# Kernel tuning notes

Hardware: AMD Instinct MI355X
Metric: run time of the kernel (lower is better)

The kernel has to match this reference:

```python
import jax, jax.numpy as jnp
import numpy as np

MARGIN = 0.2
LAMBDA_CLS = 1.0
LAMBDA_TRIPLET = 1.0
EPS = 1e-6  # matches torch pairwise_distance eps inside TripletMarginLoss
B, D, C = 8192, 192, 1024


def setup_inputs() -> dict:
    key = jax.random.key(0)
    k1, k2, k3 = jax.random.split(key, 3)
    embeddings = jax.random.normal(k1, (B, D), dtype=jnp.float32)
    logits = jax.random.normal(k2, (B, C), dtype=jnp.float32)
    targets = jax.random.randint(k3, (B,), 0, C, dtype=jnp.int64)
    return {"embeddings": embeddings, "logits": logits, "targets": targets}


def reference(embeddings, logits, targets):
    # ---- classification loss: mean cross entropy ----
    logp = jax.nn.log_softmax(logits, axis=-1)
    cls_loss = -jnp.mean(jnp.take_along_axis(logp, targets[:, None], axis=1))

    # ---- vectorized hard triplet mining (mining='hard'), on detached embeddings ----
    e = jax.lax.stop_gradient(embeddings)
    sq = jnp.sum(e * e, axis=1)                       # [B]
    d2 = sq[:, None] + sq[None, :] - 2.0 * (e @ e.T)  # [B, B]
    dist = jnp.sqrt(jnp.maximum(d2, 0.0))

    same = targets[:, None] == targets[None, :]       # [B, B]
    eye = jnp.eye(targets.shape[0], dtype=bool)
    pos_mask = same & ~eye
    neg_mask = ~same
    valid = pos_mask.any(axis=1) & neg_mask.any(axis=1)

    # hard positive: farthest same-speaker; hard negative: closest other-speaker
    pos_idx = jnp.argmax(jnp.where(pos_mask, dist, -jnp.inf), axis=1)
    neg_idx = jnp.argmin(jnp.where(neg_mask, dist, jnp.inf), axis=1)

    # ---- triplet margin loss on live embeddings ----
    a = embeddings
    p = embeddings[pos_idx]
    n = embeddings[neg_idx]
    d_ap = jnp.linalg.norm(a - p + EPS, axis=1)
    d_an = jnp.linalg.norm(a - n + EPS, axis=1)
    per_triplet = jnp.maximum(d_ap - d_an + MARGIN, 0.0)

    w = valid.astype(per_triplet.dtype)
    cnt = jnp.sum(w)
    trip_loss = jnp.where(cnt > 0, jnp.sum(per_triplet * w) / jnp.maximum(cnt, 1.0), 0.0)

    return LAMBDA_CLS * cls_loss + LAMBDA_TRIPLET * trip_loss
```

## Files before the change

kernel.cpp:

```cpp
#include <hip/hip_runtime.h>
#include <math.h>

#define B_N    8192
#define D_DIM  192
#define C_CLS  1024
#define MARGIN 0.2f
#define EPS_T  1e-6f

#define TI     128
#define TJ     128
#define JSPLIT 8
#define JLEN   (B_N / JSPLIT)
#define LDB    200

typedef short v8s  __attribute__((ext_vector_type(8)));
typedef float v16f __attribute__((ext_vector_type(16)));

__device__ __forceinline__ unsigned fkey(float f) {
  unsigned u = __float_as_uint(f);
  return (u & 0x80000000u) ? ~u : (u | 0x80000000u);
}

__device__ __forceinline__ unsigned short to_bf(float x) {
  unsigned u = __float_as_uint(x);
  u += 0x7fffu + ((u >> 16) & 1u);
  return (unsigned short)(u >> 16);
}

__global__ __launch_bounds__(256) void prep_kernel(
    const float* __restrict__ e, unsigned short* __restrict__ ebf,
    float* __restrict__ sq,
    unsigned long long* __restrict__ posw, unsigned long long* __restrict__ negw,
    float* __restrict__ accum) {
  int w = threadIdx.x >> 6, lane = threadIdx.x & 63;
  int row = blockIdx.x * 4 + w;
  const float* p = e + (size_t)row * D_DIM;
  float v0 = p[lane], v1 = p[lane + 64], v2 = p[lane + 128];
  unsigned short* q = ebf + (size_t)row * D_DIM;
  q[lane] = to_bf(v0); q[lane + 64] = to_bf(v1); q[lane + 128] = to_bf(v2);
  float s = v0 * v0 + v1 * v1 + v2 * v2;
  #pragma unroll
  for (int off = 32; off; off >>= 1) s += __shfl_xor(s, off);
  if (lane == 0) sq[row] = s;
  int b = blockIdx.x;
  if (b < 32)       posw[b * 256 + threadIdx.x] = 0ULL;
  else if (b < 64)  negw[(b - 32) * 256 + threadIdx.x] = ~0ULL;
  else if (b == 64 && threadIdx.x < 4) ((unsigned*)accum)[threadIdx.x] = 0u;
}

__global__ __launch_bounds__(256, 2) void mine_kernel(
    const unsigned short* __restrict__ ebf, const int* __restrict__ tgt,
    const float* __restrict__ sq, const float* __restrict__ logits,
    unsigned long long* __restrict__ posw, unsigned long long* __restrict__ negw,
    float* __restrict__ accum) {
  __shared__ unsigned short lds_b[TJ * LDB];
  __shared__ int   lds_t[TJ];
  __shared__ float lds_s[TJ];
  __shared__ float ce_part[4];

  const int tid  = threadIdx.x;
  const int w    = tid >> 6;
  const int lane = tid & 63;
  const int n5   = lane & 31;
  const int h    = lane >> 5;
  const int wj   = w & 1;
  const int wi   = w >> 1;
  const int i0 = blockIdx.x * TI;
  const int jb = blockIdx.y * JLEN;

  {
    const unsigned short* src = ebf + (size_t)i0 * D_DIM;
    #pragma unroll
    for (int t = 0; t < 12; ++t) {
      int c = t * 256 + tid;
      int row = c / 24;
      int off = c - row * 24;
      *(v8s*)&lds_b[row * LDB + off * 8] = *(const v8s*)(src + (size_t)row * D_DIM + off * 8);
    }
  }
  __syncthreads();
  v8s bfrag[2][12];
  #pragma unroll
  for (int tb = 0; tb < 2; ++tb)
    #pragma unroll
    for (int kc = 0; kc < 12; ++kc)
      bfrag[tb][kc] = *(const v8s*)&lds_b[(wi * 64 + tb * 32 + n5) * LDB + kc * 16 + h * 8];

  int my_t[2];
  #pragma unroll
  for (int tb = 0; tb < 2; ++tb) my_t[tb] = tgt[i0 + wi * 64 + tb * 32 + n5];

  float    pv[2] = {-3.4e38f, -3.4e38f}, nv[2] = {3.4e38f, 3.4e38f};
  unsigned pi_[2] = {0u, 0u}, ni_[2] = {0xFFFFFFFFu, 0xFFFFFFFFu};

  for (int j0 = jb; j0 < jb + JLEN; j0 += TJ) {
    __syncthreads();
    #pragma unroll
    for (int t = 0; t < 12; ++t) {
      int c = t * 256 + tid;
      int row = c / 24;
      int off = c - row * 24;
      *(v8s*)&lds_b[row * LDB + off * 8] =
          *(const v8s*)(ebf + (size_t)(j0 + row) * D_DIM + off * 8);
    }
    if (tid < TJ) { lds_t[tid] = tgt[j0 + tid]; lds_s[tid] = sq[j0 + tid]; }
    __syncthreads();

    v16f acc[2][2];
    #pragma unroll
    for (int ta = 0; ta < 2; ++ta)
      #pragma unroll
      for (int tb = 0; tb < 2; ++tb)
        #pragma unroll
        for (int r = 0; r < 16; ++r) acc[ta][tb][r] = 0.f;

    #pragma unroll
    for (int kc = 0; kc < 12; ++kc) {
      v8s afr0 = *(const v8s*)&lds_b[(wj * 64 +  0 + n5) * LDB + kc * 16 + h * 8];
      v8s afr1 = *(const v8s*)&lds_b[(wj * 64 + 32 + n5) * LDB + kc * 16 + h * 8];
      acc[0][0] = __builtin_amdgcn_mfma_f32_32x32x16_bf16(afr0, bfrag[0][kc], acc[0][0], 0, 0, 0);
      acc[0][1] = __builtin_amdgcn_mfma_f32_32x32x16_bf16(afr0, bfrag[1][kc], acc[0][1], 0, 0, 0);
      acc[1][0] = __builtin_amdgcn_mfma_f32_32x32x16_bf16(afr1, bfrag[0][kc], acc[1][0], 0, 0, 0);
      acc[1][1] = __builtin_amdgcn_mfma_f32_32x32x16_bf16(afr1, bfrag[1][kc], acc[1][1], 0, 0, 0);
    }

    #pragma unroll
    for (int ta = 0; ta < 2; ++ta)
      #pragma unroll
      for (int p = 0; p < 4; ++p) {
        int jb4 = wj * 64 + ta * 32 + p * 8 + h * 4;
        float4 s4 = *(const float4*)&lds_s[jb4];
        int4   t4 = *(const int4*)&lds_t[jb4];
        #pragma unroll
        for (int q = 0; q < 3 + 1; ++q) {
          float sv = (q == 0) ? s4.x : (q == 1) ? s4.y : (q == 2) ? s4.z : s4.w;
          int   tv = (q == 0) ? t4.x : (q == 1) ? t4.y : (q == 2) ? t4.z : t4.w;
          unsigned jg = (unsigned)(j0 + jb4 + q);
          #pragma unroll
          for (int tb = 0; tb < 2; ++tb) {
            float val = fmaf(acc[ta][tb][p * 4 + q], -2.0f, sv);
            bool same = (tv == my_t[tb]);
            float vp = same ? val : -3.4e38f;
            float vn = same ? 3.4e38f : val;
            if (vp > pv[tb]) { pv[tb] = vp; pi_[tb] = jg; }
            if (vn < nv[tb]) { nv[tb] = vn; ni_[tb] = jg; }
          }
        }
      }
  }

  #pragma unroll
  for (int tb = 0; tb < 2; ++tb) {
    unsigned long long pk =
        ((unsigned long long)fkey(pv[tb]) << 32) | (unsigned long long)(unsigned)(~pi_[tb]);
    unsigned long long nk =
        ((unsigned long long)fkey(nv[tb]) << 32) | (unsigned long long)ni_[tb];
    unsigned long long po = __shfl_xor(pk, 32);
    unsigned long long no = __shfl_xor(nk, 32);
    pk = pk > po ? pk : po;
    nk = nk < no ? nk : no;
    if (h == 0) {
      int irow = i0 + wi * 64 + tb * 32 + n5;
      atomicMax(&posw[irow], pk);
      atomicMin(&negw[irow], nk);
    }
  }

  int blin = blockIdx.y * 64 + blockIdx.x;
  float ce_acc = 0.f;
  #pragma unroll
  for (int it = 0; it < 4; ++it) {
    int row = blin * 16 + it * 4 + w;
    const float* lp = logits + (size_t)row * C_CLS;
    float4 x[4];
    #pragma unroll
    for (int t = 0; t < 4; ++t) x[t] = *(const float4*)(lp + lane * 4 + 256 * t);
    float m = -3.4e38f;
    #pragma unroll
    for (int t = 0; t < 4; ++t)
      m = fmaxf(m, fmaxf(fmaxf(x[t].x, x[t].y), fmaxf(x[t].z, x[t].w)));
    #pragma unroll
    for (int off = 32; off; off >>= 1) m = fmaxf(m, __shfl_xor(m, off));
    float s = 0.f;
    #pragma unroll
    for (int t = 0; t < 4; ++t)
      s += __expf(x[t].x - m) + __expf(x[t].y - m) +
           __expf(x[t].z - m) + __expf(x[t].w - m);
    #pragma unroll
    for (int off = 32; off; off >>= 1) s += __shfl_xor(s, off);
    if (lane == 0) ce_acc += m + __logf(s) - lp[tgt[row]];
  }
  if (lane == 0) ce_part[w] = ce_acc;
  __syncthreads();
  if (tid == 0)
    atomicAdd(&accum[0], ce_part[0] + ce_part[1] + ce_part[2] + ce_part[3]);
}

__global__ __launch_bounds__(1024) void trip_fin_kernel(
    const float* __restrict__ e,
    const unsigned long long* __restrict__ posw,
    const unsigned long long* __restrict__ negw,
    float* __restrict__ accum, float* __restrict__ out) {
  __shared__ float ssum[16];
  __shared__ float scnt[16];
  int w = threadIdx.x >> 6, lane = threadIdx.x & 63;
  int i = blockIdx.x * 16 + w;
  unsigned long long pp = posw[i], np = negw[i];
  unsigned pidx = ~(unsigned)pp;
  unsigned nidx = (unsigned)np;
  float res = 0.f, c = 0.f;
  if (pp != 0ULL && np != ~0ULL && pidx != (unsigned)i) {
    const float* pa = e + (size_t)i * D_DIM;
    const float* pb = e + (size_t)pidx * D_DIM;
    const float* pc = e + (size_t)nidx * D_DIM;
    float dap = 0.f, dan = 0.f;
    #pragma unroll
    for (int t = 0; t < 3; ++t) {
      int k = lane + 64 * t;
      float av = pa[k];
      float d1 = av - pb[k] + EPS_T;
      float d2 = av - pc[k] + EPS_T;
      dap += d1 * d1;
      dan += d2 * d2;
    }
    #pragma unroll
    for (int off = 32; off; off >>= 1) {
      dap += __shfl_xor(dap, off);
      dan += __shfl_xor(dan, off);
    }
    res = fmaxf(sqrtf(dap) - sqrtf(dan) + MARGIN, 0.f);
    c = 1.f;
  }
  if (lane == 0) { ssum[w] = res; scnt[w] = c; }
  __syncthreads();
  if (threadIdx.x == 0) {
    float a = 0.f, b = 0.f;
    #pragma unroll
    for (int k = 0; k < 16; ++k) { a += ssum[k]; b += scnt[k]; }
    atomicAdd(&accum[1], a);
    atomicAdd(&accum[2], b);
    __threadfence();
    unsigned old = atomicAdd((unsigned*)&accum[3], 1u);
    if (old == 511u) {
      __threadfence();
      float cls = atomicAdd(&accum[0], 0.f);
      float ts  = atomicAdd(&accum[1], 0.f);
      float tc  = atomicAdd(&accum[2], 0.f);
      float trip = (tc > 0.f) ? ts / fmaxf(tc, 1.f) : 0.f;
      out[0] = cls / (float)B_N + trip;
    }
  }
}

extern "C" void kernel_launch(void* const* d_in, const int* in_sizes, int n_in,
                              void* d_out, int out_size, void* d_ws, size_t ws_size,
                              hipStream_t stream) {
  const float* emb    = (const float*)d_in[0];
  const float* logits = (const float*)d_in[1];
  const int*   tgt    = (const int*)d_in[2];
  float* out = (float*)d_out;

  char* ws = (char*)d_ws;
  unsigned short* ebf = (unsigned short*)ws;
  unsigned long long* posw = (unsigned long long*)(ws + 3145728);
  unsigned long long* negw = (unsigned long long*)(ws + 3145728 + 65536);
  float* sq    = (float*)(ws + 3145728 + 131072);
  float* accum = (float*)(ws + 3145728 + 163840);

  prep_kernel<<<2048, 256, 0, stream>>>(emb, ebf, sq, posw, negw, accum);
  mine_kernel<<<dim3(B_N / TI, JSPLIT), 256, 0, stream>>>(ebf, tgt, sq, logits, posw, negw, accum);
  trip_fin_kernel<<<512, 1024, 0, stream>>>(emb, posw, negw, accum, out);
}
```

Measured before the change: 147.7 us.

## Shrink mining tile to 64 rows, double j-split, merge argmax via LDS atomics

Mining now uses 64 anchor rows per block, with all four waves sharing the same anchor fragments, and the j range is split 16 ways instead of 8. This doubles the grid to 2048 blocks and raises the occupancy target to 3 blocks per CU. Per-row pos/neg results are first merged in shared memory with LDS atomics, so each block issues one global atomic per row. The cross-entropy work is redistributed to one row per wave. The trade-off is lower MFMA reuse per B-tile load: each 128-row j tile now feeds only 64 anchors, which doubles total L2 traffic for the j tiles.

```diff
diff --git a/kernel.cpp b/kernel.cpp
--- a/kernel.cpp
+++ b/kernel.cpp
@@ -7,9 +7,9 @@
 #define MARGIN 0.2f
 #define EPS_T  1e-6f
 
-#define TI     128
+#define TI     64
 #define TJ     128
-#define JSPLIT 8
+#define JSPLIT 16
 #define JLEN   (B_N / JSPLIT)
 #define LDB    200
 
@@ -48,7 +48,7 @@
   else if (b == 64 && threadIdx.x < 4) ((unsigned*)accum)[threadIdx.x] = 0u;
 }
 
-__global__ __launch_bounds__(256, 2) void mine_kernel(
+__global__ __launch_bounds__(256, 3) void mine_kernel(
     const unsigned short* __restrict__ ebf, const int* __restrict__ tgt,
     const float* __restrict__ sq, const float* __restrict__ logits,
     unsigned long long* __restrict__ posw, unsigned long long* __restrict__ negw,
@@ -56,6 +56,8 @@
   __shared__ unsigned short lds_b[TJ * LDB];
   __shared__ int   lds_t[TJ];
   __shared__ float lds_s[TJ];
+  __shared__ unsigned long long pmrg[TI];
+  __shared__ unsigned long long nmrg[TI];
   __shared__ float ce_part[4];
 
   const int tid  = threadIdx.x;
@@ -63,15 +65,15 @@
   const int lane = tid & 63;
   const int n5   = lane & 31;
   const int h    = lane >> 5;
-  const int wj   = w & 1;
-  const int wi   = w >> 1;
   const int i0 = blockIdx.x * TI;
   const int jb = blockIdx.y * JLEN;
 
+  if (tid < TI) { pmrg[tid] = 0ULL; nmrg[tid] = ~0ULL; }
+
   {
     const unsigned short* src = ebf + (size_t)i0 * D_DIM;
     #pragma unroll
-    for (int t = 0; t < 12; ++t) {
+    for (int t = 0; t < 6; ++t) {
       int c = t * 256 + tid;
       int row = c / 24;
       int off = c - row * 24;
@@ -84,11 +86,11 @@
   for (int tb = 0; tb < 2; ++tb)
     #pragma unroll
     for (int kc = 0; kc < 12; ++kc)
-      bfrag[tb][kc] = *(const v8s*)&lds_b[(wi * 64 + tb * 32 + n5) * LDB + kc * 16 + h * 8];
+      bfrag[tb][kc] = *(const v8s*)&lds_b[(tb * 32 + n5) * LDB + kc * 16 + h * 8];
 
   int my_t[2];
   #pragma unroll
-  for (int tb = 0; tb < 2; ++tb) my_t[tb] = tgt[i0 + wi * 64 + tb * 32 + n5];
+  for (int tb = 0; tb < 2; ++tb) my_t[tb] = tgt[i0 + tb * 32 + n5];
 
   float    pv[2] = {-3.4e38f, -3.4e38f}, nv[2] = {3.4e38f, 3.4e38f};
   unsigned pi_[2] = {0u, 0u}, ni_[2] = {0xFFFFFFFFu, 0xFFFFFFFFu};
@@ -106,47 +108,40 @@
     if (tid < TJ) { lds_t[tid] = tgt[j0 + tid]; lds_s[tid] = sq[j0 + tid]; }
     __syncthreads();
 
-    v16f acc[2][2];
-    #pragma unroll
-    for (int ta = 0; ta < 2; ++ta)
+    v16f acc[2];
+    #pragma unroll
+    for (int tb = 0; tb < 2; ++tb)
       #pragma unroll
-      for (int tb = 0; tb < 2; ++tb)
+      for (int r = 0; r < 16; ++r) acc[tb][r] = 0.f;
+
+    #pragma unroll
+    for (int kc = 0; kc < 12; ++kc) {
+      v8s afr = *(const v8s*)&lds_b[(w * 32 + n5) * LDB + kc * 16 + h * 8];
+      acc[0] = __builtin_amdgcn_mfma_f32_32x32x16_bf16(afr, bfrag[0][kc], acc[0], 0, 0, 0);
+      acc[1] = __builtin_amdgcn_mfma_f32_32x32x16_bf16(afr, bfrag[1][kc], acc[1], 0, 0, 0);
+    }
+
+    #pragma unroll
+    for (int p = 0; p < 4; ++p) {
+      int jb4 = w * 32 + p * 8 + h * 4;
+      float4 s4 = *(const float4*)&lds_s[jb4];
+      int4   t4 = *(const int4*)&lds_t[jb4];
+      #pragma unroll
+      for (int q = 0; q < 4; ++q) {
+        float sv = (q == 0) ? s4.x : (q == 1) ? s4.y : (q == 2) ? s4.z : s4.w;
+        int   tv = (q == 0) ? t4.x : (q == 1) ? t4.y : (q == 2) ? t4.z : t4.w;
+        unsigned jg = (unsigned)(j0 + jb4 + q);
         #pragma unroll
-        for (int r = 0; r < 16; ++r) acc[ta][tb][r] = 0.f;
-
-    #pragma unroll
-    for (int kc = 0; kc < 12; ++kc) {
-      v8s afr0 = *(const v8s*)&lds_b[(wj * 64 +  0 + n5) * LDB + kc * 16 + h * 8];
-      v8s afr1 = *(const v8s*)&lds_b[(wj * 64 + 32 + n5) * LDB + kc * 16 + h * 8];
-      acc[0][0] = __builtin_amdgcn_mfma_f32_32x32x16_bf16(afr0, bfrag[0][kc], acc[0][0], 0, 0, 0);
-      acc[0][1] = __builtin_amdgcn_mfma_f32_32x32x16_bf16(afr0, bfrag[1][kc], acc[0][1], 0, 0, 0);
-      acc[1][0] = __builtin_amdgcn_mfma_f32_32x32x16_bf16(afr1, bfrag[0][kc], acc[1][0], 0, 0, 0);
-      acc[1][1] = __builtin_amdgcn_mfma_f32_32x32x16_bf16(afr1, bfrag[1][kc], acc[1][1], 0, 0, 0);
-    }
-
-    #pragma unroll
-    for (int ta = 0; ta < 2; ++ta)
-      #pragma unroll
-      for (int p = 0; p < 4; ++p) {
-        int jb4 = wj * 64 + ta * 32 + p * 8 + h * 4;
-        float4 s4 = *(const float4*)&lds_s[jb4];
-        int4   t4 = *(const int4*)&lds_t[jb4];
-        #pragma unroll
-        for (int q = 0; q < 3 + 1; ++q) {
-          float sv = (q == 0) ? s4.x : (q == 1) ? s4.y : (q == 2) ? s4.z : s4.w;
-          int   tv = (q == 0) ? t4.x : (q == 1) ? t4.y : (q == 2) ? t4.z : t4.w;
-          unsigned jg = (unsigned)(j0 + jb4 + q);
-          #pragma unroll
-          for (int tb = 0; tb < 2; ++tb) {
-            float val = fmaf(acc[ta][tb][p * 4 + q], -2.0f, sv);
-            bool same = (tv == my_t[tb]);
-            float vp = same ? val : -3.4e38f;
-            float vn = same ? 3.4e38f : val;
-            if (vp > pv[tb]) { pv[tb] = vp; pi_[tb] = jg; }
-            if (vn < nv[tb]) { nv[tb] = vn; ni_[tb] = jg; }
-          }
+        for (int tb = 0; tb < 2; ++tb) {
+          float val = fmaf(acc[tb][p * 4 + q], -2.0f, sv);
+          bool same = (tv == my_t[tb]);
+          float vp = same ? val : -3.4e38f;
+          float vn = same ? 3.4e38f : val;
+          if (vp > pv[tb]) { pv[tb] = vp; pi_[tb] = jg; }
+          if (vn < nv[tb]) { nv[tb] = vn; ni_[tb] = jg; }
         }
       }
+    }
   }
 
   #pragma unroll
@@ -160,17 +155,18 @@
     pk = pk > po ? pk : po;
     nk = nk < no ? nk : no;
     if (h == 0) {
-      int irow = i0 + wi * 64 + tb * 32 + n5;
-      atomicMax(&posw[irow], pk);
-      atomicMin(&negw[irow], nk);
-    }
-  }
-
-  int blin = blockIdx.y * 64 + blockIdx.x;
-  float ce_acc = 0.f;
-  #pragma unroll
-  for (int it = 0; it < 4; ++it) {
-    int row = blin * 16 + it * 4 + w;
+      atomicMax(&pmrg[tb * 32 + n5], pk);
+      atomicMin(&nmrg[tb * 32 + n5], nk);
+    }
+  }
+  __syncthreads();
+  if (tid < TI) {
+    atomicMax(&posw[i0 + tid], pmrg[tid]);
+    atomicMin(&negw[i0 + tid], nmrg[tid]);
+  }
+
+  {
+    int row = (blockIdx.y * 128 + blockIdx.x) * 4 + w;
     const float* lp = logits + (size_t)row * C_CLS;
     float4 x[4];
     #pragma unroll
@@ -188,9 +184,8 @@
            __expf(x[t].z - m) + __expf(x[t].w - m);
     #pragma unroll
     for (int off = 32; off; off >>= 1) s += __shfl_xor(s, off);
-    if (lane == 0) ce_acc += m + __logf(s) - lp[tgt[row]];
-  }
-  if (lane == 0) ce_part[w] = ce_acc;
+    if (lane == 0) ce_part[w] = m + __logf(s) - lp[tgt[row]];
+  }
   __syncthreads();
   if (tid == 0)
     atomicAdd(&accum[0], ce_part[0] + ce_part[1] + ce_part[2] + ce_part[3]);
```

Result: slower. 215.9 us (+46.2%).

## Stage embedding tiles via direct global-to-LDS loads with XOR-swizzled layout

Applied to the files above, without the earlier changes.

Embedding tiles are now copied from global memory straight into LDS using global_load_lds DMA instead of going through registers. The LDS layout changes to 512-byte rows with an XOR swizzle to avoid bank conflicts. The block's whole sq and target slice is preloaded once instead of per tile. The mining compare is rewritten to use predicated updates. This cuts VGPR traffic and per-tile load instructions, but there is still no double buffering, and the swizzle and padding logic adds address math and risk.

```diff
diff --git a/kernel.cpp b/kernel.cpp
--- a/kernel.cpp
+++ b/kernel.cpp
@@ -11,10 +11,33 @@
 #define TJ     128
 #define JSPLIT 8
 #define JLEN   (B_N / JSPLIT)
-#define LDB    200
+#define NT     (JLEN / TJ)
+#define RB     512
 
 typedef short v8s  __attribute__((ext_vector_type(8)));
 typedef float v16f __attribute__((ext_vector_type(16)));
+
+typedef __attribute__((address_space(3))) unsigned int       lds_u32;
+typedef __attribute__((address_space(1))) const unsigned int glb_u32;
+
+__device__ __forceinline__ void gll16(const void* g, void* l) {
+  __builtin_amdgcn_global_load_lds((glb_u32*)g, (lds_u32*)l, 16, 0, 0);
+}
+
+__device__ __forceinline__ int swz(int r, int s) {
+  return r * RB + ((s ^ (r & 31)) << 4);
+}
+
+__device__ __forceinline__ void stage_tile(char* dst, const char* src, int tid) {
+  #pragma unroll
+  for (int k = 0; k < 16; ++k) {
+    int c = k * 256 + tid;
+    int r = c >> 5;
+    int s = (c & 31) ^ (r & 31);
+    int so = (s < 24) ? (s << 4) : 0;
+    gll16(src + r * 384 + so, dst + (k * 256 + (tid & ~63)) * 16);
+  }
+}
 
 __device__ __forceinline__ unsigned fkey(float f) {
   unsigned u = __float_as_uint(f);
@@ -53,9 +76,9 @@
     const float* __restrict__ sq, const float* __restrict__ logits,
     unsigned long long* __restrict__ posw, unsigned long long* __restrict__ negw,
     float* __restrict__ accum) {
-  __shared__ unsigned short lds_b[TJ * LDB];
-  __shared__ int   lds_t[TJ];
-  __shared__ float lds_s[TJ];
+  __shared__ unsigned short lds_b[TJ * (RB / 2)];
+  __shared__ float lds_sq[JLEN];
+  __shared__ int   lds_tg[JLEN];
   __shared__ float ce_part[4];
 
   const int tid  = threadIdx.x;
@@ -68,42 +91,31 @@
   const int i0 = blockIdx.x * TI;
   const int jb = blockIdx.y * JLEN;
 
-  {
-    const unsigned short* src = ebf + (size_t)i0 * D_DIM;
-    #pragma unroll
-    for (int t = 0; t < 12; ++t) {
-      int c = t * 256 + tid;
-      int row = c / 24;
-      int off = c - row * 24;
-      *(v8s*)&lds_b[row * LDB + off * 8] = *(const v8s*)(src + (size_t)row * D_DIM + off * 8);
-    }
-  }
+  char* ldsc = (char*)lds_b;
+
+  stage_tile(ldsc, (const char*)(ebf + (size_t)i0 * D_DIM), tid);
+  gll16((const char*)(sq  + jb) + tid * 16, (char*)lds_sq + (tid & ~63) * 16);
+  gll16((const char*)(tgt + jb) + tid * 16, (char*)lds_tg + (tid & ~63) * 16);
+
+  int my_t[2];
+  #pragma unroll
+  for (int tb = 0; tb < 2; ++tb) my_t[tb] = tgt[i0 + wi * 64 + tb * 32 + n5];
+
   __syncthreads();
+
   v8s bfrag[2][12];
   #pragma unroll
   for (int tb = 0; tb < 2; ++tb)
     #pragma unroll
     for (int kc = 0; kc < 12; ++kc)
-      bfrag[tb][kc] = *(const v8s*)&lds_b[(wi * 64 + tb * 32 + n5) * LDB + kc * 16 + h * 8];
-
-  int my_t[2];
-  #pragma unroll
-  for (int tb = 0; tb < 2; ++tb) my_t[tb] = tgt[i0 + wi * 64 + tb * 32 + n5];
+      bfrag[tb][kc] = *(const v8s*)(ldsc + swz(wi * 64 + tb * 32 + n5, 2 * kc + h));
 
   float    pv[2] = {-3.4e38f, -3.4e38f}, nv[2] = {3.4e38f, 3.4e38f};
   unsigned pi_[2] = {0u, 0u}, ni_[2] = {0xFFFFFFFFu, 0xFFFFFFFFu};
 
-  for (int j0 = jb; j0 < jb + JLEN; j0 += TJ) {
+  for (int t = 0; t < NT; ++t) {
     __syncthreads();
-    #pragma unroll
-    for (int t = 0; t < 12; ++t) {
-      int c = t * 256 + tid;
-      int row = c / 24;
-      int off = c - row * 24;
-      *(v8s*)&lds_b[row * LDB + off * 8] =
-          *(const v8s*)(ebf + (size_t)(j0 + row) * D_DIM + off * 8);
-    }
-    if (tid < TJ) { lds_t[tid] = tgt[j0 + tid]; lds_s[tid] = sq[j0 + tid]; }
+    stage_tile(ldsc, (const char*)(ebf + (size_t)(jb + t * TJ) * D_DIM), tid);
     __syncthreads();
 
     v16f acc[2][2];
@@ -116,23 +128,25 @@
 
     #pragma unroll
     for (int kc = 0; kc < 12; ++kc) {
-      v8s afr0 = *(const v8s*)&lds_b[(wj * 64 +  0 + n5) * LDB + kc * 16 + h * 8];
-      v8s afr1 = *(const v8s*)&lds_b[(wj * 64 + 32 + n5) * LDB + kc * 16 + h * 8];
+      v8s afr0 = *(const v8s*)(ldsc + swz(wj * 64 +  0 + n5, 2 * kc + h));
+      v8s afr1 = *(const v8s*)(ldsc + swz(wj * 64 + 32 + n5, 2 * kc + h));
       acc[0][0] = __builtin_amdgcn_mfma_f32_32x32x16_bf16(afr0, bfrag[0][kc], acc[0][0], 0, 0, 0);
       acc[0][1] = __builtin_amdgcn_mfma_f32_32x32x16_bf16(afr0, bfrag[1][kc], acc[0][1], 0, 0, 0);
       acc[1][0] = __builtin_amdgcn_mfma_f32_32x32x16_bf16(afr1, bfrag[0][kc], acc[1][0], 0, 0, 0);
       acc[1][1] = __builtin_amdgcn_mfma_f32_32x32x16_bf16(afr1, bfrag[1][kc], acc[1][1], 0, 0, 0);
     }
 
+    const int j0 = jb + t * TJ;
+    const int jt = t * TJ;
     #pragma unroll
     for (int ta = 0; ta < 2; ++ta)
       #pragma unroll
       for (int p = 0; p < 4; ++p) {
         int jb4 = wj * 64 + ta * 32 + p * 8 + h * 4;
-        float4 s4 = *(const float4*)&lds_s[jb4];
-        int4   t4 = *(const int4*)&lds_t[jb4];
+        float4 s4 = *(const float4*)&lds_sq[jt + jb4];
+        int4   t4 = *(const int4*)&lds_tg[jt + jb4];
         #pragma unroll
-        for (int q = 0; q < 3 + 1; ++q) {
+        for (int q = 0; q < 4; ++q) {
           float sv = (q == 0) ? s4.x : (q == 1) ? s4.y : (q == 2) ? s4.z : s4.w;
           int   tv = (q == 0) ? t4.x : (q == 1) ? t4.y : (q == 2) ? t4.z : t4.w;
           unsigned jg = (unsigned)(j0 + jb4 + q);
@@ -140,10 +154,8 @@
           for (int tb = 0; tb < 2; ++tb) {
             float val = fmaf(acc[ta][tb][p * 4 + q], -2.0f, sv);
             bool same = (tv == my_t[tb]);
-            float vp = same ? val : -3.4e38f;
-            float vn = same ? 3.4e38f : val;
-            if (vp > pv[tb]) { pv[tb] = vp; pi_[tb] = jg; }
-            if (vn < nv[tb]) { nv[tb] = vn; ni_[tb] = jg; }
+            if (same  && val > pv[tb]) { pv[tb] = val; pi_[tb] = jg; }
+            if (!same && val < nv[tb]) { nv[tb] = val; ni_[tb] = jg; }
           }
         }
       }
@@ -166,31 +178,33 @@
     }
   }
 
-  int blin = blockIdx.y * 64 + blockIdx.x;
-  float ce_acc = 0.f;
-  #pragma unroll
-  for (int it = 0; it < 4; ++it) {
-    int row = blin * 16 + it * 4 + w;
-    const float* lp = logits + (size_t)row * C_CLS;
-    float4 x[4];
-    #pragma unroll
-    for (int t = 0; t < 4; ++t) x[t] = *(const float4*)(lp + lane * 4 + 256 * t);
-    float m = -3.4e38f;
-    #pragma unroll
-    for (int t = 0; t < 4; ++t)
-      m = fmaxf(m, fmaxf(fmaxf(x[t].x, x[t].y), fmaxf(x[t].z, x[t].w)));
-    #pragma unroll
-    for (int off = 32; off; off >>= 1) m = fmaxf(m, __shfl_xor(m, off));
-    float s = 0.f;
-    #pragma unroll
-    for (int t = 0; t < 4; ++t)
-      s += __expf(x[t].x - m) + __expf(x[t].y - m) +
-           __expf(x[t].z - m) + __expf(x[t].w - m);
-    #pragma unroll
-    for (int off = 32; off; off >>= 1) s += __shfl_xor(s, off);
-    if (lane == 0) ce_acc += m + __logf(s) - lp[tgt[row]];
-  }
-  if (lane == 0) ce_part[w] = ce_acc;
+  {
+    int blin = blockIdx.y * 64 + blockIdx.x;
+    float ce_acc = 0.f;
+    #pragma unroll
+    for (int it = 0; it < 4; ++it) {
+      int row = blin * 16 + it * 4 + w;
+      const float* lp = logits + (size_t)row * C_CLS;
+      float4 x[4];
+      #pragma unroll
+      for (int u = 0; u < 4; ++u) x[u] = *(const float4*)(lp + lane * 4 + 256 * u);
+      float m = -3.4e38f;
+      #pragma unroll
+      for (int u = 0; u < 4; ++u)
+        m = fmaxf(m, fmaxf(fmaxf(x[u].x, x[u].y), fmaxf(x[u].z, x[u].w)));
+      #pragma unroll
+      for (int off = 32; off; off >>= 1) m = fmaxf(m, __shfl_xor(m, off));
+      float s = 0.f;
+      #pragma unroll
+      for (int u = 0; u < 4; ++u)
+        s += __expf(x[u].x - m) + __expf(x[u].y - m) +
+             __expf(x[u].z - m) + __expf(x[u].w - m);
+      #pragma unroll
+      for (int off = 32; off; off >>= 1) s += __shfl_xor(s, off);
+      if (lane == 0) ce_acc += m + __logf(s) - lp[tgt[row]];
+    }
+    if (lane == 0) ce_part[w] = ce_acc;
+  }
   __syncthreads();
   if (tid == 0)
     atomicAdd(&accum[0], ce_part[0] + ce_part[1] + ce_part[2] + ce_part[3]);
```

New measurement: 157.1 us. 6.4% more time.
